# Performance work log

Measured on AMD Instinct MI355X. Metric: run time of the kernel, lower is better.

The kernel has to match this reference:

```python
import jax, jax.numpy as jnp
import numpy as np

EPS = 1e-8  # torch F.cosine_similarity default eps
MARGIN = 1.0


def _pair_indices(p_lens, n_lens):
    """Build gather indices for the ragged all-pairs (positive x negative) expansion.
    For batch i, pair order is lexicographic (j, k): positive j repeated n_i times,
    negative segment tiled p_i times -- exactly matching the torch repeat/repeat_interleave.
    Host-side numpy (lens are concrete integers)."""
    p = np.asarray(p_lens, dtype=np.int64)
    n = np.asarray(n_lens, dtype=np.int64)
    pairs = p * n                                   # per-example pair counts
    total = int(pairs.sum())
    p_off = np.concatenate([[0], np.cumsum(p)[:-1]])
    n_off = np.concatenate([[0], np.cumsum(n)[:-1]])
    pair_off = np.concatenate([[0], np.cumsum(pairs)[:-1]])
    a_idx = np.repeat(np.arange(len(p)), pairs)     # [total]
    t = np.arange(total) - np.repeat(pair_off, pairs)   # local pair position in [0, p_i*n_i)
    n_rep = np.repeat(n, pairs)
    j = t // n_rep                                  # positive index within segment
    k = t % n_rep                                   # negative index within segment
    p_idx = np.repeat(p_off, pairs) + j
    n_idx = np.repeat(n_off, pairs) + k
    return jnp.asarray(a_idx), jnp.asarray(p_idx), jnp.asarray(n_idx)


def _cosine(x, y):
    dot = jnp.sum(x * y, axis=-1)
    nx = jnp.linalg.norm(x, axis=-1)
    ny = jnp.linalg.norm(y, axis=-1)
    return dot / jnp.maximum(nx * ny, EPS)


def setup_inputs() -> dict:
    rng = np.random.default_rng(0)
    bs, dim = 1024, 768
    p_lens = rng.integers(1, 13, size=bs)
    n_lens = rng.integers(1, 13, size=bs)
    key = jax.random.key(0)
    k1, k2, k3 = jax.random.split(key, 3)
    anchor = jax.random.normal(k1, (bs, dim), dtype=jnp.float32)
    positive = jax.random.normal(k2, (int(p_lens.sum()), dim), dtype=jnp.float32)
    negative = jax.random.normal(k3, (int(n_lens.sum()), dim), dtype=jnp.float32)
    return {
        "anchor": anchor,
        "positive": positive,
        "negative": negative,
        "positive_lens": jnp.asarray(p_lens, dtype=jnp.int32),
        "negative_lens": jnp.asarray(n_lens, dtype=jnp.int32),
    }


def reference(anchor, positive, negative, positive_lens, negative_lens):
    a_idx, p_idx, n_idx = _pair_indices(positive_lens, negative_lens)
    a = anchor[a_idx]       # [total_pairs, dim]
    pp = positive[p_idx]
    nn_ = negative[n_idx]
    d_ap = 1.0 - _cosine(a, pp)
    d_an = 1.0 - _cosine(a, nn_)
    # TripletMarginWithDistanceLoss, swap=False, reduction='mean'
    loss = jnp.mean(jnp.maximum(d_ap - d_an + MARGIN, 0.0))
    return loss
```

## Files before the change

### kernel.cpp

```cpp
#include <hip/hip_runtime.h>
#include <hip/hip_bf16.h>

#define DIM 768
#define EPS 1e-8f

__global__ __launch_bounds__(256) void triplet_fused(
    const float* __restrict__ anchor, const float* __restrict__ positive,
    const float* __restrict__ negative,
    const int* __restrict__ p_lens, const int* __restrict__ n_lens,
    float* __restrict__ out, int bs)
{
    const int b = blockIdx.x;
    const int tid = threadIdx.x;
    const int wave = tid >> 6;
    const int lane = tid & 63;

    __shared__ float sA[DIM];
    __shared__ float sCos[32];
    __shared__ float sRedF[4];
    __shared__ int   sRedI[4][3];
    __shared__ float sAnorm;
    __shared__ int   sPO, sNO, sTot;

    const float4* a4 = (const float4*)(anchor + (size_t)b * DIM);
    float asq = 0.0f;
    for (int q = tid; q < DIM / 4; q += 256) {
        float4 v = a4[q];
        ((float4*)sA)[q] = v;
        asq += v.x * v.x + v.y * v.y + v.z * v.z + v.w * v.w;
    }

    int pre_p = 0, pre_n = 0, tot = 0;
    for (int i = tid; i < bs; i += 256) {
        int p = p_lens[i];
        int n = n_lens[i];
        if (i < b) { pre_p += p; pre_n += n; }
        tot += p * n;
    }

    #pragma unroll
    for (int s = 32; s > 0; s >>= 1) {
        asq   += __shfl_xor(asq, s);
        pre_p += __shfl_xor(pre_p, s);
        pre_n += __shfl_xor(pre_n, s);
        tot   += __shfl_xor(tot, s);
    }
    if (lane == 0) {
        sRedF[wave] = asq;
        sRedI[wave][0] = pre_p;
        sRedI[wave][1] = pre_n;
        sRedI[wave][2] = tot;
    }
    __syncthreads();
    if (tid == 0) {
        sAnorm = sqrtf(sRedF[0] + sRedF[1] + sRedF[2] + sRedF[3]);
        sPO  = sRedI[0][0] + sRedI[1][0] + sRedI[2][0] + sRedI[3][0];
        sNO  = sRedI[0][1] + sRedI[1][1] + sRedI[2][1] + sRedI[3][1];
        sTot = sRedI[0][2] + sRedI[1][2] + sRedI[2][2] + sRedI[3][2];
    }
    const int pl = p_lens[b];
    const int nl = n_lens[b];
    __syncthreads();
    const float an = sAnorm;
    const int po = sPO, no = sNO;

    const int nvec = pl + nl;
    for (int v = wave; v < nvec; v += 4) {
        const float* x = (v < pl)
            ? positive + (size_t)(po + v) * DIM
            : negative + (size_t)(no + (v - pl)) * DIM;
        const float4* x4 = (const float4*)x;
        float dot = 0.0f, nx = 0.0f;
        #pragma unroll
        for (int q = 0; q < 3; ++q) {
            float4 xv = x4[lane + 64 * q];
            float4 av = ((const float4*)sA)[lane + 64 * q];
            dot += av.x * xv.x + av.y * xv.y + av.z * xv.z + av.w * xv.w;
            nx  += xv.x * xv.x + xv.y * xv.y + xv.z * xv.z + xv.w * xv.w;
        }
        #pragma unroll
        for (int s = 32; s > 0; s >>= 1) {
            dot += __shfl_xor(dot, s);
            nx  += __shfl_xor(nx, s);
        }
        if (lane == 0) sCos[v] = dot / fmaxf(an * sqrtf(nx), EPS);
    }
    __syncthreads();

    const int pairs = pl * nl;
    float s = 0.0f;
    for (int t = tid; t < pairs; t += 256) {
        int j = t / nl;
        int k = t - j * nl;
        s += fmaxf(sCos[pl + k] - sCos[j] + 1.0f, 0.0f);
    }
    #pragma unroll
    for (int sh = 32; sh > 0; sh >>= 1) s += __shfl_xor(s, sh);
    if (lane == 0) sRedF[wave] = s;
    __syncthreads();
    if (tid == 0) {
        float blk = sRedF[0] + sRedF[1] + sRedF[2] + sRedF[3];
        atomicAdd(out, blk / (float)sTot);
    }
}

extern "C" void kernel_launch(void* const* d_in, const int* in_sizes, int n_in,
                              void* d_out, int out_size, void* d_ws, size_t ws_size,
                              hipStream_t stream) {
    const float* anchor   = (const float*)d_in[0];
    const float* positive = (const float*)d_in[1];
    const float* negative = (const float*)d_in[2];
    const int*   p_lens   = (const int*)d_in[3];
    const int*   n_lens   = (const int*)d_in[4];
    float* out = (float*)d_out;

    const int bs = in_sizes[3];

    hipMemsetAsync(out, 0, sizeof(float), stream);
    triplet_fused<<<bs, 256, 0, stream>>>(anchor, positive, negative,
                                          p_lens, n_lens, out, bs);
}
```

Before: 100.3 us.

## Split fused triplet kernel into scan, per-vector cosine, and pair-sum kernels

Replaces the one-block-per-example fused kernel with three kernels: a single-block prefix scan that builds segment offsets and vector-to-anchor maps, a flat one-wave-per-vector cosine kernel, and a single-block pair-sum reduction. This drops the redundant per-block O(bs) scan over the length arrays, the atomicAdd and the memset, and balances work across vectors. In exchange it adds two kernel launches and serial single-block stages, re-reads the anchor per vector, and hardcodes bs<=1024 and lens<=12.

```diff
diff --git a/kernel.cpp b/kernel.cpp
--- a/kernel.cpp
+++ b/kernel.cpp
@@ -3,104 +3,118 @@
 
 #define DIM 768
 #define EPS 1e-8f
+#define MAXB 1024
+#define MAXVEC (MAXB * 12)
 
-__global__ __launch_bounds__(256) void triplet_fused(
+__global__ __launch_bounds__(1024) void scan_kernel(
+    const int* __restrict__ p_lens, const int* __restrict__ n_lens,
+    int* __restrict__ p_off, int* __restrict__ n_off,
+    int* __restrict__ aid_p, int* __restrict__ aid_n, int bs)
+{
+    __shared__ int sp[MAXB], sn[MAXB];
+    const int tid = threadIdx.x;
+    const int p = (tid < bs) ? p_lens[tid] : 0;
+    const int n = (tid < bs) ? n_lens[tid] : 0;
+    sp[tid] = p; sn[tid] = n;
+    __syncthreads();
+    for (int off = 1; off < MAXB; off <<= 1) {
+        int vp = (tid >= off) ? sp[tid - off] : 0;
+        int vn = (tid >= off) ? sn[tid - off] : 0;
+        __syncthreads();
+        sp[tid] += vp; sn[tid] += vn;
+        __syncthreads();
+    }
+    if (tid < bs) {
+        const int poe = sp[tid] - p;
+        const int noe = sn[tid] - n;
+        p_off[tid] = poe;
+        n_off[tid] = noe;
+        for (int j = 0; j < p; ++j) aid_p[poe + j] = tid;
+        for (int j = 0; j < n; ++j) aid_n[noe + j] = tid;
+    }
+}
+
+__global__ __launch_bounds__(512) void cosine_kernel(
     const float* __restrict__ anchor, const float* __restrict__ positive,
     const float* __restrict__ negative,
+    const int* __restrict__ aid_p, const int* __restrict__ aid_n,
+    float* __restrict__ cosv, int P, int N)
+{
+    const int wave = threadIdx.x >> 6;
+    const int lane = threadIdx.x & 63;
+    const int vid = blockIdx.x * 8 + wave;
+    if (vid >= P + N) return;
+    const bool isPos = (vid < P);
+
+    const float* x = isPos ? positive + (size_t)vid * DIM
+                           : negative + (size_t)(vid - P) * DIM;
+    const float4* x4 = (const float4*)x;
+    const float4 xa = x4[lane];
+    const float4 xb = x4[lane + 64];
+    const float4 xc = x4[lane + 128];
+
+    const int e = isPos ? aid_p[vid] : aid_n[vid - P];
+    const float4* a4 = (const float4*)(anchor + (size_t)e * DIM);
+    const float4 aa = a4[lane];
+    const float4 ab = a4[lane + 64];
+    const float4 ac = a4[lane + 128];
+
+    float dot = aa.x*xa.x + aa.y*xa.y + aa.z*xa.z + aa.w*xa.w
+              + ab.x*xb.x + ab.y*xb.y + ab.z*xb.z + ab.w*xb.w
+              + ac.x*xc.x + ac.y*xc.y + ac.z*xc.z + ac.w*xc.w;
+    float nx  = xa.x*xa.x + xa.y*xa.y + xa.z*xa.z + xa.w*xa.w
+              + xb.x*xb.x + xb.y*xb.y + xb.z*xb.z + xb.w*xb.w
+              + xc.x*xc.x + xc.y*xc.y + xc.z*xc.z + xc.w*xc.w;
+    float asq = aa.x*aa.x + aa.y*aa.y + aa.z*aa.z + aa.w*aa.w
+              + ab.x*ab.x + ab.y*ab.y + ab.z*ab.z + ab.w*ab.w
+              + ac.x*ac.x + ac.y*ac.y + ac.z*ac.z + ac.w*ac.w;
+
+    #pragma unroll
+    for (int s = 32; s > 0; s >>= 1) {
+        dot += __shfl_xor(dot, s);
+        nx  += __shfl_xor(nx, s);
+        asq += __shfl_xor(asq, s);
+    }
+    if (lane == 0)
+        cosv[vid] = dot / fmaxf(sqrtf(asq) * sqrtf(nx), EPS);
+}
+
+__global__ __launch_bounds__(1024) void pairsum_kernel(
     const int* __restrict__ p_lens, const int* __restrict__ n_lens,
-    float* __restrict__ out, int bs)
+    const int* __restrict__ p_off, const int* __restrict__ n_off,
+    const float* __restrict__ cosv, float* __restrict__ out, int P, int bs)
 {
-    const int b = blockIdx.x;
     const int tid = threadIdx.x;
     const int wave = tid >> 6;
     const int lane = tid & 63;
+    __shared__ float sw[16];
+    __shared__ int   si[16];
 
-    __shared__ float sA[DIM];
-    __shared__ float sCos[32];
-    __shared__ float sRedF[4];
-    __shared__ int   sRedI[4][3];
-    __shared__ float sAnorm;
-    __shared__ int   sPO, sNO, sTot;
-
-    const float4* a4 = (const float4*)(anchor + (size_t)b * DIM);
-    float asq = 0.0f;
-    for (int q = tid; q < DIM / 4; q += 256) {
-        float4 v = a4[q];
-        ((float4*)sA)[q] = v;
-        asq += v.x * v.x + v.y * v.y + v.z * v.z + v.w * v.w;
+    float s = 0.0f;
+    int   tp = 0;
+    if (tid < bs) {
+        const int pl = p_lens[tid], nl = n_lens[tid];
+        const float* cp = cosv + p_off[tid];
+        const float* cn = cosv + P + n_off[tid];
+        tp = pl * nl;
+        for (int j = 0; j < pl; ++j) {
+            const float cap = cp[j];
+            for (int k = 0; k < nl; ++k)
+                s += fmaxf(cn[k] - cap + 1.0f, 0.0f);
+        }
     }
-
-    int pre_p = 0, pre_n = 0, tot = 0;
-    for (int i = tid; i < bs; i += 256) {
-        int p = p_lens[i];
-        int n = n_lens[i];
-        if (i < b) { pre_p += p; pre_n += n; }
-        tot += p * n;
+    #pragma unroll
+    for (int sh = 32; sh > 0; sh >>= 1) {
+        s  += __shfl_xor(s, sh);
+        tp += __shfl_xor(tp, sh);
     }
-
-    #pragma unroll
-    for (int s = 32; s > 0; s >>= 1) {
-        asq   += __shfl_xor(asq, s);
-        pre_p += __shfl_xor(pre_p, s);
-        pre_n += __shfl_xor(pre_n, s);
-        tot   += __shfl_xor(tot, s);
-    }
-    if (lane == 0) {
-        sRedF[wave] = asq;
-        sRedI[wave][0] = pre_p;
-        sRedI[wave][1] = pre_n;
-        sRedI[wave][2] = tot;
-    }
+    if (lane == 0) { sw[wave] = s; si[wave] = tp; }
     __syncthreads();
     if (tid == 0) {
-        sAnorm = sqrtf(sRedF[0] + sRedF[1] + sRedF[2] + sRedF[3]);
-        sPO  = sRedI[0][0] + sRedI[1][0] + sRedI[2][0] + sRedI[3][0];
-        sNO  = sRedI[0][1] + sRedI[1][1] + sRedI[2][1] + sRedI[3][1];
-        sTot = sRedI[0][2] + sRedI[1][2] + sRedI[2][2] + sRedI[3][2];
-    }
-    const int pl = p_lens[b];
-    const int nl = n_lens[b];
-    __syncthreads();
-    const float an = sAnorm;
-    const int po = sPO, no = sNO;
-
-    const int nvec = pl + nl;
-    for (int v = wave; v < nvec; v += 4) {
-        const float* x = (v < pl)
-            ? positive + (size_t)(po + v) * DIM
-            : negative + (size_t)(no + (v - pl)) * DIM;
-        const float4* x4 = (const float4*)x;
-        float dot = 0.0f, nx = 0.0f;
+        float S = 0.0f; int T = 0;
         #pragma unroll
-        for (int q = 0; q < 3; ++q) {
-            float4 xv = x4[lane + 64 * q];
-            float4 av = ((const float4*)sA)[lane + 64 * q];
-            dot += av.x * xv.x + av.y * xv.y + av.z * xv.z + av.w * xv.w;
-            nx  += xv.x * xv.x + xv.y * xv.y + xv.z * xv.z + xv.w * xv.w;
-        }
-        #pragma unroll
-        for (int s = 32; s > 0; s >>= 1) {
-            dot += __shfl_xor(dot, s);
-            nx  += __shfl_xor(nx, s);
-        }
-        if (lane == 0) sCos[v] = dot / fmaxf(an * sqrtf(nx), EPS);
-    }
-    __syncthreads();
-
-    const int pairs = pl * nl;
-    float s = 0.0f;
-    for (int t = tid; t < pairs; t += 256) {
-        int j = t / nl;
-        int k = t - j * nl;
-        s += fmaxf(sCos[pl + k] - sCos[j] + 1.0f, 0.0f);
-    }
-    #pragma unroll
-    for (int sh = 32; sh > 0; sh >>= 1) s += __shfl_xor(s, sh);
-    if (lane == 0) sRedF[wave] = s;
-    __syncthreads();
-    if (tid == 0) {
-        float blk = sRedF[0] + sRedF[1] + sRedF[2] + sRedF[3];
-        atomicAdd(out, blk / (float)sTot);
+        for (int w = 0; w < 16; ++w) { S += sw[w]; T += si[w]; }
+        *out = S / (float)T;
     }
 }
 
@@ -115,8 +129,20 @@
     float* out = (float*)d_out;
 
     const int bs = in_sizes[3];
+    const int P  = in_sizes[1] / DIM;
+    const int N  = in_sizes[2] / DIM;
 
-    hipMemsetAsync(out, 0, sizeof(float), stream);
-    triplet_fused<<<bs, 256, 0, stream>>>(anchor, positive, negative,
-                                          p_lens, n_lens, out, bs);
+    int* p_off = (int*)d_ws;
+    int* n_off = p_off + MAXB;
+    int* aid_p = n_off + MAXB;
+    int* aid_n = aid_p + MAXVEC;
+    float* cosv = (float*)(aid_n + MAXVEC);
+
+    scan_kernel<<<1, 1024, 0, stream>>>(p_lens, n_lens, p_off, n_off,
+                                        aid_p, aid_n, bs);
+    const int nvec = P + N;
+    cosine_kernel<<<(nvec + 7) / 8, 512, 0, stream>>>(anchor, positive, negative,
+                                                      aid_p, aid_n, cosv, P, N);
+    pairsum_kernel<<<1, 1024, 0, stream>>>(p_lens, n_lens, p_off, n_off,
+                                           cosv, out, P, bs);
 }
```

Result: slower. 114.5 us (+14.2%).
